# Performance work log

Hardware: AMD Instinct MI355X
Metric: run time of the kernel (lower is better)

## Reference

```python
import jax, jax.numpy as jnp
import numpy as np

E = 1024   # embed_dim
H = 16     # num_heads
D = E // H # head_dim
M = 2048   # query length
N = 2048   # key/value length
B = 4      # batch
SCALE = 1.0 / float(np.sqrt(D))


def setup_inputs() -> dict:
    key = jax.random.key(0)
    ks = jax.random.split(key, 11)
    s = 0.02
    return {
        "query": jax.random.normal(ks[0], (M, B, E), jnp.float32),
        "key": jax.random.normal(ks[1], (N, B, E), jnp.float32),
        "value": jax.random.normal(ks[2], (N, B, E), jnp.float32),
        "Wq": jax.random.normal(ks[3], (E, E), jnp.float32) * s,
        "bq": jax.random.normal(ks[4], (E,), jnp.float32) * s,
        "Wk": jax.random.normal(ks[5], (E, E), jnp.float32) * s,
        "bk": jax.random.normal(ks[6], (E,), jnp.float32) * s,
        "Wv": jax.random.normal(ks[7], (E, E), jnp.float32) * s,
        "bv": jax.random.normal(ks[8], (E,), jnp.float32) * s,
        "Wo": jax.random.normal(ks[9], (E, E), jnp.float32) * s,
        "bo": jax.random.normal(ks[10], (E,), jnp.float32) * s,
    }


def reference(query, key, value, Wq, bq, Wk, bk, Wv, bv, Wo, bo):
    # batch_first=False: (M,B,E) -> (B,M,E)
    q = jnp.swapaxes(query, 0, 1)
    k = jnp.swapaxes(key, 0, 1)
    v = jnp.swapaxes(value, 0, 1)
    # projections (torch Linear: x @ W^T + b; here W stored as (in,out))
    q = (q @ Wq + bq).reshape(B, M, H, D)
    k = (k @ Wk + bk).reshape(B, N, H, D)
    v = (v @ Wv + bv).reshape(B, N, H, D)
    # per-head attention, vectorized over heads (same math as the Python loop)
    logits = jnp.einsum("bmhd,bnhd->bhmn", q, k) * SCALE
    attn = jax.nn.softmax(logits, axis=-1)
    out = jnp.einsum("bhmn,bnhd->bmhd", attn, v).reshape(B, M, E)
    out = out @ Wo + bo
    # back to (M,B,E)
    return jnp.swapaxes(out, 0, 1)
```

## Files before the change

kernel.cpp:

```cpp
#include <hip/hip_runtime.h>

typedef unsigned short u16;
typedef unsigned int u32;
typedef __bf16 bf16x8 __attribute__((ext_vector_type(8)));
typedef float f32x4 __attribute__((ext_vector_type(4)));
typedef float f32x16 __attribute__((ext_vector_type(16)));
typedef unsigned short u16x8 __attribute__((ext_vector_type(8)));
typedef unsigned short u16x4 __attribute__((ext_vector_type(4)));

#define LOG2E 1.44269504088896f

__device__ __forceinline__ float fast_exp2(float x) {
#if __has_builtin(__builtin_amdgcn_exp2f)
  return __builtin_amdgcn_exp2f(x);
#else
  return exp2f(x);
#endif
}

__device__ __forceinline__ u16 f2bf(float x) {
  union { __bf16 b; u16 u; } c;
  c.b = (__bf16)x;
  return c.u;
}

__device__ __forceinline__ u32 cvtpk_bf16(float lo_, float hi_) {
  u32 r;
  asm("v_cvt_pk_bf16_f32 %0, %1, %2" : "=v"(r) : "v"(lo_), "v"(hi_));
  return r;
}

__device__ __forceinline__ void permswap32(u32& a, u32& b) {
  asm volatile("v_permlane32_swap_b32 %0, %1" : "+v"(a), "+v"(b));
}

__device__ __forceinline__ void gload_lds16(const void* g, void* l) {
  __builtin_amdgcn_global_load_lds(
      (__attribute__((address_space(1))) void*)(g),
      (__attribute__((address_space(3))) void*)(l), 16, 0, 0);
}

__device__ __forceinline__ int swz_off(int row, int col) {
  return row * 64 + ((((col >> 3) ^ (row ^ (row >> 3))) & 7) << 3) + (col & 7);
}

__global__ __launch_bounds__(256) void transpose_cvt4(
    const float* __restrict__ Wq, const float* __restrict__ Wk,
    const float* __restrict__ Wv, const float* __restrict__ Wo,
    u16* __restrict__ Wqt, u16* __restrict__ Wkt,
    u16* __restrict__ Wvt, u16* __restrict__ Wot) {
  const int E = 1024;
  const float* W = blockIdx.z == 0 ? Wq : blockIdx.z == 1 ? Wk
                   : blockIdx.z == 2 ? Wv : Wo;
  u16* Wt = blockIdx.z == 0 ? Wqt : blockIdx.z == 1 ? Wkt
            : blockIdx.z == 2 ? Wvt : Wot;
  __shared__ float tile[32][33];
  int tx = threadIdx.x & 31, ty = threadIdx.x >> 5;
  int bx = blockIdx.x * 32, by = blockIdx.y * 32;
  #pragma unroll
  for (int i = 0; i < 32; i += 8)
    tile[ty + i][tx] = W[(size_t)(by + ty + i) * E + bx + tx];
  __syncthreads();
  #pragma unroll
  for (int i = 0; i < 32; i += 8)
    Wt[(size_t)(bx + ty + i) * E + by + tx] = f2bf(tile[tx][ty + i]);
}

__global__ __launch_bounds__(256) void proj_qkv(
    const float* __restrict__ Xq, const float* __restrict__ Xk,
    const float* __restrict__ Xv,
    const u16* __restrict__ Wqt, const u16* __restrict__ Wkt,
    const u16* __restrict__ Wvt,
    const float* __restrict__ bq, const float* __restrict__ bk,
    const float* __restrict__ bv,
    u16* __restrict__ Qp, u16* __restrict__ Kp, u16* __restrict__ Vp,
    float qscale)
{
  constexpr int K = 1024, N = 1024;
  const float* A; const u16* Bt; const float* bias; u16* C; float oscale;
  if (blockIdx.z == 0)      { A = Xq; Bt = Wqt; bias = bq; C = Qp; oscale = qscale; }
  else if (blockIdx.z == 1) { A = Xk; Bt = Wkt; bias = bk; C = Kp; oscale = 1.f; }
  else                      { A = Xv; Bt = Wvt; bias = bv; C = Vp; oscale = 1.f; }

  __shared__ u16 As[128 * 64];
  __shared__ u16 Bs[128 * 64];
  const int tid = threadIdx.x;
  const int w = tid >> 6;
  const int lane = tid & 63;
  const int lo = lane & 15, hi = lane >> 4;
  const int brow = blockIdx.x * 128;
  const int bcol = blockIdx.y * 128;
  const int wr = (w >> 1) * 64;
  const int wc = (w & 1) * 64;

  f32x4 acc[4][4] = {};

  for (int k0 = 0; k0 < K; k0 += 64) {
    __syncthreads();
    #pragma unroll
    for (int i = 0; i < 4; i++) {
      int c = i * 256 + tid;
      int rowo = c >> 3;
      int ko = (c & 7) * 8;
      gload_lds16(Bt + (size_t)(bcol + rowo) * K + k0 + ko,
                  (void*)(Bs + (size_t)(i * 256 + w * 64) * 8));
    }
    #pragma unroll
    for (int i = 0; i < 4; i++) {
      int c = i * 256 + tid;
      int rowo = c >> 3;
      int ko = (c & 7) * 8;
      const float* Ap = A + (size_t)(brow + rowo) * K + k0 + ko;
      float4 v0 = *(const float4*)Ap;
      float4 v1 = *(const float4*)(Ap + 4);
      u16x8 ab;
      ab[0] = f2bf(v0.x); ab[1] = f2bf(v0.y); ab[2] = f2bf(v0.z); ab[3] = f2bf(v0.w);
      ab[4] = f2bf(v1.x); ab[5] = f2bf(v1.y); ab[6] = f2bf(v1.z); ab[7] = f2bf(v1.w);
      *(u16x8*)(As + swz_off(rowo, ko)) = ab;
    }
    __syncthreads();
    #pragma unroll
    for (int kk = 0; kk < 2; kk++) {
      bf16x8 af[4], bfr[4];
      #pragma unroll
      for (int mi = 0; mi < 4; mi++)
        af[mi] = *(const bf16x8*)(As + swz_off(wr + mi * 16 + lo, kk * 32 + hi * 8));
      #pragma unroll
      for (int ni = 0; ni < 4; ni++)
        bfr[ni] = *(const bf16x8*)(Bs + (wc + ni * 16 + lo) * 64 + kk * 32 + hi * 8);
      #pragma unroll
      for (int mi = 0; mi < 4; mi++)
        #pragma unroll
        for (int ni = 0; ni < 4; ni++)
          acc[mi][ni] = __builtin_amdgcn_mfma_f32_16x16x32_bf16(
              af[mi], bfr[ni], acc[mi][ni], 0, 0, 0);
    }
  }

  #pragma unroll
  for (int mi = 0; mi < 4; mi++)
    #pragma unroll
    for (int ni = 0; ni < 4; ni++) {
      int row = brow + wr + mi * 16 + hi * 4;
      int col = bcol + wc + ni * 16 + lo;
      float bv = bias[col];
      #pragma unroll
      for (int r = 0; r < 4; r++) {
        float v = (acc[mi][ni][r] + bv) * oscale;
        C[(size_t)(row + r) * N + col] = f2bf(v);
      }
    }
}

__global__ __launch_bounds__(256) void gemm_out(
    const u16* __restrict__ A, const u16* __restrict__ Bt,
    const float* __restrict__ bias, float* __restrict__ C)
{
  constexpr int K = 1024, N = 1024;
  __shared__ u16 As[128 * 64];
  __shared__ u16 Bs[128 * 64];
  const int tid = threadIdx.x;
  const int w = tid >> 6;
  const int lane = tid & 63;
  const int lo = lane & 15, hi = lane >> 4;
  const int brow = blockIdx.x * 128;
  const int bcol = blockIdx.y * 128;
  const int wr = (w >> 1) * 64;
  const int wc = (w & 1) * 64;

  f32x4 acc[4][4] = {};

  for (int k0 = 0; k0 < K; k0 += 64) {
    __syncthreads();
    #pragma unroll
    for (int i = 0; i < 4; i++) {
      int c = i * 256 + tid;
      int rowo = c >> 3;
      int ko = (c & 7) * 8;
      gload_lds16(A + (size_t)(brow + rowo) * K + k0 + ko,
                  (void*)(As + (size_t)(i * 256 + w * 64) * 8));
      gload_lds16(Bt + (size_t)(bcol + rowo) * K + k0 + ko,
                  (void*)(Bs + (size_t)(i * 256 + w * 64) * 8));
    }
    __syncthreads();
    #pragma unroll
    for (int kk = 0; kk < 2; kk++) {
      bf16x8 af[4], bfr[4];
      #pragma unroll
      for (int mi = 0; mi < 4; mi++)
        af[mi] = *(const bf16x8*)(As + (wr + mi * 16 + lo) * 64 + kk * 32 + hi * 8);
      #pragma unroll
      for (int ni = 0; ni < 4; ni++)
        bfr[ni] = *(const bf16x8*)(Bs + (wc + ni * 16 + lo) * 64 + kk * 32 + hi * 8);
      #pragma unroll
      for (int mi = 0; mi < 4; mi++)
        #pragma unroll
        for (int ni = 0; ni < 4; ni++)
          acc[mi][ni] = __builtin_amdgcn_mfma_f32_16x16x32_bf16(
              af[mi], bfr[ni], acc[mi][ni], 0, 0, 0);
    }
  }

  #pragma unroll
  for (int mi = 0; mi < 4; mi++)
    #pragma unroll
    for (int ni = 0; ni < 4; ni++) {
      int row = brow + wr + mi * 16 + hi * 4;
      int col = bcol + wc + ni * 16 + lo;
      float bv = bias[col];
      #pragma unroll
      for (int r = 0; r < 4; r++)
        C[(size_t)(row + r) * N + col] = acc[mi][ni][r] + bv;
    }
}

__global__ __launch_bounds__(256) void attn_kernel(
    const u16* __restrict__ Qp, const u16* __restrict__ Kp,
    const u16* __restrict__ Vp, u16* __restrict__ O)
{
  constexpr int Bb = 4, E = 1024, Nn = 2048;
  constexpr int NT = Nn / 64;
  __shared__ u16 Ks[2][64 * 64];
  __shared__ u16 Vt[2][64 * 64];

  const int tid = threadIdx.x;
  const int lane = tid & 63;
  const int w = tid >> 6;
  const int l31 = lane & 31;
  const int hi5 = lane >> 5;

  const int wg = blockIdx.x;
  const int swz = (wg & 7) * 128 + (wg >> 3);
  const int b_ = swz >> 8;
  const int h = (swz >> 4) & 15;
  const int mbase = (swz & 15) * 128 + w * 32;
  const int m = mbase + l31;

  bf16x8 q[4];
  {
    const u16* qrow = Qp + (size_t)(m * Bb + b_) * E + h * 64;
    #pragma unroll
    for (int kb = 0; kb < 4; kb++)
      q[kb] = *(const bf16x8*)(qrow + kb * 16 + hi5 * 8);
  }

  f32x16 oacc[2] = {};
  float lrun = 0.f;

  const int nrK = tid >> 3;
  const int q8K = (tid & 7) * 8;
  const int dq = (tid & 15) * 4;
  const int nq = (tid >> 4) * 4;
  const size_t rstride = (size_t)Bb * E;
  const size_t KSTEP = 64 * rstride;
  const u16* kpt = Kp + (size_t)nrK * rstride + (size_t)b_ * E + h * 64 + q8K;
  const u16* vpt = Vp + (size_t)nq * rstride + (size_t)b_ * E + h * 64 + dq;

  u16x8 kreg[2];
  u16x4 vreg[4];
  kreg[0] = *(const u16x8*)(kpt);
  kreg[1] = *(const u16x8*)(kpt + 32 * rstride);
  #pragma unroll
  for (int j = 0; j < 4; j++)
    vreg[j] = *(const u16x4*)(vpt + j * rstride);
  kpt += KSTEP; vpt += KSTEP;

  int it = 0;
  for (int t = 0; t < NT; t++, it ^= 1) {
    #pragma unroll
    for (int i = 0; i < 2; i++)
      *(u16x8*)(&Ks[it][swz_off(i * 32 + nrK, q8K)]) = kreg[i];
    #pragma unroll
    for (int jw = 0; jw < 4; jw++) {
      u16x4 colv;
      #pragma unroll
      for (int j = 0; j < 4; j++) colv[j] = vreg[j][jw];
      *(u16x4*)(&Vt[it][swz_off(dq + jw, nq)]) = colv;
    }
    __syncthreads();
    if (t < NT - 1) {
      kreg[0] = *(const u16x8*)(kpt);
      kreg[1] = *(const u16x8*)(kpt + 32 * rstride);
      #pragma unroll
      for (int j = 0; j < 4; j++)
        vreg[j] = *(const u16x4*)(vpt + j * rstride);
      kpt += KSTEP; vpt += KSTEP;
    }
    const u16* ksp = &Ks[it][0];
    const u16* vtp = &Vt[it][0];

    f32x16 st[2];
    __builtin_amdgcn_s_setprio(1);
    #pragma unroll
    for (int sb = 0; sb < 2; sb++) {
      f32x16 tacc = {};
      #pragma unroll
      for (int kb = 0; kb < 4; kb++) {
        bf16x8 kf = *(const bf16x8*)(ksp + swz_off(sb * 32 + l31, kb * 16 + hi5 * 8));
        tacc = __builtin_amdgcn_mfma_f32_32x32x16_bf16(kf, q[kb], tacc, 0, 0, 0);
      }
      st[sb] = tacc;
    }
    __builtin_amdgcn_s_setprio(0);

    u32 pk[2][8];
    float ra = 0.f, rb = 0.f, rc = 0.f, rd = 0.f;
    #pragma unroll
    for (int sb = 0; sb < 2; sb++) {
      #pragma unroll
      for (int j = 0; j < 8; j++) {
        float p0 = fast_exp2(st[sb][2 * j]);
        float p1 = fast_exp2(st[sb][2 * j + 1]);
        if (j & 1) { ra += p0; rb += p1; } else { rc += p0; rd += p1; }
        pk[sb][j] = cvtpk_bf16(p0, p1);
      }
    }
    lrun += (ra + rb) + (rc + rd);

    bf16x8 pb[4];
    #pragma unroll
    for (int kb = 0; kb < 4; kb++) {
      int sb = kb >> 1, c = kb & 1;
      u32 a0 = pk[sb][4 * c + 0], b0 = pk[sb][4 * c + 2];
      u32 a1 = pk[sb][4 * c + 1], b1 = pk[sb][4 * c + 3];
      permswap32(a0, b0);
      permswap32(a1, b1);
      union { u32 d[4]; bf16x8 v; } u;
      u.d[0] = a0; u.d[1] = a1; u.d[2] = b0; u.d[3] = b1;
      pb[kb] = u.v;
    }

    __builtin_amdgcn_s_setprio(1);
    #pragma unroll
    for (int dsb = 0; dsb < 2; dsb++) {
      #pragma unroll
      for (int kb = 0; kb < 4; kb++) {
        bf16x8 vf = *(const bf16x8*)(vtp + swz_off(dsb * 32 + l31, kb * 16 + hi5 * 8));
        oacc[dsb] = __builtin_amdgcn_mfma_f32_32x32x16_bf16(vf, pb[kb], oacc[dsb], 0, 0, 0);
      }
    }
    __builtin_amdgcn_s_setprio(0);
  }

  float l = lrun + __shfl_xor(lrun, 32);
  float inv = 1.f / l;
  u16* orow = O + (size_t)(m * Bb + b_) * E + h * 64;
  #pragma unroll
  for (int dsb = 0; dsb < 2; dsb++) {
    #pragma unroll
    for (int qd = 0; qd < 4; qd++) {
      u16x4 o;
      #pragma unroll
      for (int t = 0; t < 4; t++) o[t] = f2bf(oacc[dsb][qd * 4 + t] * inv);
      *(u16x4*)(orow + dsb * 32 + qd * 8 + hi5 * 4) = o;
    }
  }
}

extern "C" void kernel_launch(void* const* d_in, const int* in_sizes, int n_in,
                              void* d_out, int out_size, void* d_ws, size_t ws_size,
                              hipStream_t stream) {
  const float* query = (const float*)d_in[0];
  const float* key   = (const float*)d_in[1];
  const float* value = (const float*)d_in[2];
  const float* Wq = (const float*)d_in[3];
  const float* bq = (const float*)d_in[4];
  const float* Wk = (const float*)d_in[5];
  const float* bk = (const float*)d_in[6];
  const float* Wv = (const float*)d_in[7];
  const float* bv = (const float*)d_in[8];
  const float* Wo = (const float*)d_in[9];
  const float* bo = (const float*)d_in[10];
  float* out = (float*)d_out;

  const float QSCALE = 0.125f * LOG2E;

  const size_t XE = (size_t)2048 * 4 * 1024;
  const size_t WE = (size_t)1024 * 1024;
  u16* ws  = (u16*)d_ws;
  u16* Qp  = ws;
  u16* Kp  = Qp + XE;
  u16* Vp  = Kp + XE;
  u16* Ob  = Vp + XE;
  u16* Wqt = Ob + XE;
  u16* Wkt = Wqt + WE;
  u16* Wvt = Wkt + WE;
  u16* Wot = Wvt + WE;

  dim3 blk(256);
  transpose_cvt4<<<dim3(32, 32, 4), blk, 0, stream>>>(
      Wq, Wk, Wv, Wo, Wqt, Wkt, Wvt, Wot);

  proj_qkv<<<dim3(64, 8, 3), blk, 0, stream>>>(
      query, key, value, Wqt, Wkt, Wvt, bq, bk, bv, Qp, Kp, Vp, QSCALE);

  attn_kernel<<<1024, blk, 0, stream>>>(Qp, Kp, Vp, Ob);

  gemm_out<<<dim3(64, 8), blk, 0, stream>>>(Ob, Wot, bo, out);
}
```

Measured before the change: 219.5 us.

## Software-pipeline QKV projection with register prefetch and double-buffered weight tiles

The QKV projection GEMM now loads the next K-tile of fp32 activations into registers and issues the next weight tile's global-to-LDS copy into a second LDS buffer before running the MFMAs on the current tile. This is meant to hide global memory latency behind matrix math instead of serialising load, convert and compute each iteration. It costs extra LDS for the second weight buffer and 32 more registers per thread for the prefetched activations, which may lower occupancy.

```diff
diff --git a/kernel.cpp b/kernel.cpp
--- a/kernel.cpp
+++ b/kernel.cpp
@@ -76,14 +76,14 @@
     u16* __restrict__ Qp, u16* __restrict__ Kp, u16* __restrict__ Vp,
     float qscale)
 {
-  constexpr int K = 1024, N = 1024;
+  constexpr int K = 1024, N = 1024, NT = K / 64;
   const float* A; const u16* Bt; const float* bias; u16* C; float oscale;
   if (blockIdx.z == 0)      { A = Xq; Bt = Wqt; bias = bq; C = Qp; oscale = qscale; }
   else if (blockIdx.z == 1) { A = Xk; Bt = Wkt; bias = bk; C = Kp; oscale = 1.f; }
   else                      { A = Xv; Bt = Wvt; bias = bv; C = Vp; oscale = 1.f; }
 
   __shared__ u16 As[128 * 64];
-  __shared__ u16 Bs[128 * 64];
+  __shared__ u16 Bs[2][128 * 64];
   const int tid = threadIdx.x;
   const int w = tid >> 6;
   const int lane = tid & 63;
@@ -92,33 +92,51 @@
   const int bcol = blockIdx.y * 128;
   const int wr = (w >> 1) * 64;
   const int wc = (w & 1) * 64;
+  const int rowt = tid >> 3;
+  const int ko = (tid & 7) * 8;
 
   f32x4 acc[4][4] = {};
 
-  for (int k0 = 0; k0 < K; k0 += 64) {
+  float4 a0[4], a1[4];
+  #pragma unroll
+  for (int i = 0; i < 4; i++) {
+    const float* Ap = A + (size_t)(brow + i * 32 + rowt) * K + ko;
+    a0[i] = *(const float4*)Ap;
+    a1[i] = *(const float4*)(Ap + 4);
+  }
+  #pragma unroll
+  for (int i = 0; i < 4; i++)
+    gload_lds16(Bt + (size_t)(bcol + i * 32 + rowt) * K + ko,
+                (void*)(Bs[0] + (size_t)(i * 256 + w * 64) * 8));
+
+  int cur = 0;
+  for (int t = 0; t < NT; t++) {
+    #pragma unroll
+    for (int i = 0; i < 4; i++) {
+      u16x8 ab;
+      ab[0] = f2bf(a0[i].x); ab[1] = f2bf(a0[i].y);
+      ab[2] = f2bf(a0[i].z); ab[3] = f2bf(a0[i].w);
+      ab[4] = f2bf(a1[i].x); ab[5] = f2bf(a1[i].y);
+      ab[6] = f2bf(a1[i].z); ab[7] = f2bf(a1[i].w);
+      *(u16x8*)(As + swz_off(i * 32 + rowt, ko)) = ab;
+    }
     __syncthreads();
-    #pragma unroll
-    for (int i = 0; i < 4; i++) {
-      int c = i * 256 + tid;
-      int rowo = c >> 3;
-      int ko = (c & 7) * 8;
-      gload_lds16(Bt + (size_t)(bcol + rowo) * K + k0 + ko,
-                  (void*)(Bs + (size_t)(i * 256 + w * 64) * 8));
-    }
-    #pragma unroll
-    for (int i = 0; i < 4; i++) {
-      int c = i * 256 + tid;
-      int rowo = c >> 3;
-      int ko = (c & 7) * 8;
-      const float* Ap = A + (size_t)(brow + rowo) * K + k0 + ko;
-      float4 v0 = *(const float4*)Ap;
-      float4 v1 = *(const float4*)(Ap + 4);
-      u16x8 ab;
-      ab[0] = f2bf(v0.x); ab[1] = f2bf(v0.y); ab[2] = f2bf(v0.z); ab[3] = f2bf(v0.w);
-      ab[4] = f2bf(v1.x); ab[5] = f2bf(v1.y); ab[6] = f2bf(v1.z); ab[7] = f2bf(v1.w);
-      *(u16x8*)(As + swz_off(rowo, ko)) = ab;
-    }
-    __syncthreads();
+
+    if (t + 1 < NT) {
+      const int k0n = (t + 1) * 64;
+      #pragma unroll
+      for (int i = 0; i < 4; i++) {
+        const float* Ap = A + (size_t)(brow + i * 32 + rowt) * K + k0n + ko;
+        a0[i] = *(const float4*)Ap;
+        a1[i] = *(const float4*)(Ap + 4);
+      }
+      #pragma unroll
+      for (int i = 0; i < 4; i++)
+        gload_lds16(Bt + (size_t)(bcol + i * 32 + rowt) * K + k0n + ko,
+                    (void*)(Bs[cur ^ 1] + (size_t)(i * 256 + w * 64) * 8));
+    }
+
+    const u16* bsp = Bs[cur];
     #pragma unroll
     for (int kk = 0; kk < 2; kk++) {
       bf16x8 af[4], bfr[4];
@@ -127,7 +145,7 @@
         af[mi] = *(const bf16x8*)(As + swz_off(wr + mi * 16 + lo, kk * 32 + hi * 8));
       #pragma unroll
       for (int ni = 0; ni < 4; ni++)
-        bfr[ni] = *(const bf16x8*)(Bs + (wc + ni * 16 + lo) * 64 + kk * 32 + hi * 8);
+        bfr[ni] = *(const bf16x8*)(bsp + (wc + ni * 16 + lo) * 64 + kk * 32 + hi * 8);
       #pragma unroll
       for (int mi = 0; mi < 4; mi++)
         #pragma unroll
@@ -135,6 +153,8 @@
           acc[mi][ni] = __builtin_amdgcn_mfma_f32_16x16x32_bf16(
               af[mi], bfr[ni], acc[mi][ni], 0, 0, 0);
     }
+    __syncthreads();
+    cur ^= 1;
   }
 
   #pragma unroll
```

New measurement: 236.2 us. 1.08x slower.
